# Optimization experiments

Hardware: AMD Instinct MI355X
Metric: run time of the kernel (lower is better)

The kernel has to match this reference:

```python
import jax, jax.numpy as jnp
import numpy as np

B, C, H, W = 16, 1024, 64, 64
NODE_H, NODE_W = 32, 32
N = NODE_H * NODE_W          # 1024 nodes
HID = 16                     # hidden_ch


def setup_inputs() -> dict:
    key = jax.random.key(0)
    k0, k1, k2 = jax.random.split(key, 3)
    feature = jax.random.normal(k0, (B, C, H, W), dtype=jnp.float32)
    mu_w = jax.random.normal(k1, (HID, C, 3, 3), dtype=jnp.float32) * 0.02
    mu_b = jnp.zeros((HID,), dtype=jnp.float32)
    lv_w = jax.random.normal(k2, (HID, C, 1, 1), dtype=jnp.float32) * 0.02
    lv_b = jnp.zeros((HID,), dtype=jnp.float32)
    return {"feature": feature, "mu_w": mu_w, "mu_b": mu_b, "lv_w": lv_w, "lv_b": lv_b}


def _conv(x, w, b, pad):
    y = jax.lax.conv_general_dilated(
        x, w, window_strides=(1, 1), padding=pad,
        dimension_numbers=("NCHW", "OIHW", "NCHW"))
    return y + b[None, :, None, None]


def reference(feature, mu_w, mu_b, lv_w, lv_b):
    # AdaptiveAvgPool2d((32,32)) with H,W multiples of 32 == mean over 2x2 blocks
    nodes = feature.reshape(B, C, NODE_H, H // NODE_H, NODE_W, W // NODE_W).mean(axis=(3, 5))
    mu = _conv(nodes, mu_w, mu_b, "SAME")      # (B, HID, 32, 32), Dropout is identity at eval
    log_var = _conv(nodes, lv_w, lv_b, "VALID")  # 1x1 conv, pad 0

    # eval-mode reparameterize: z = mu; torch raw reshape (B,HID,32,32)->(B,N,HID)
    z = mu.reshape(B, N, HID)

    kl_loss = -(0.5 * N * HID) * jnp.mean(
        jnp.sum(1.0 + 2.0 * log_var - mu ** 2 - jnp.exp(log_var) ** 2, axis=1))

    A = jnp.einsum("bnc,bmc->bnm", z, z)       # (B, N, N)
    A = jax.nn.relu(A)
    Ad = jnp.diagonal(A, axis1=1, axis2=2)      # (B, N)
    sigma = jnp.sum(Ad, axis=1)                 # (B,)
    gamma = jnp.sqrt(1.0 + N / (sigma + 1e-7))[:, None, None]  # (B,1,1)
    dl_loss = -gamma * jnp.log(Ad + 1e-7).sum() / (B * N * N)  # (B,1,1), faithful to torch

    eye = jnp.eye(N, dtype=A.dtype)
    A = A + gamma * (Ad[:, :, None] * eye)      # batched diagflat scatter

    # Laplacian normalize with self loop
    A = A + eye[None]
    deg_inv_sqrt = (jnp.sum(A, axis=1) + 1e-5) ** -0.5          # (B, N)
    LA = deg_inv_sqrt[:, :, None] * A * deg_inv_sqrt[:, None, :]

    z_hat = mu.reshape(B, N, HID) * (1.0 - log_var.reshape(B, N, HID))
    z_hat = gamma * z_hat
    return (LA, z, z_hat, kl_loss, dl_loss)
```

## Files before the change

kernel.cpp:

```cpp
#include <hip/hip_runtime.h>

typedef short short8 __attribute__((ext_vector_type(8)));
typedef float f32x4 __attribute__((ext_vector_type(4)));
typedef unsigned short ushort4v __attribute__((ext_vector_type(4)));

#define ZOFF   16777216
#define ZHOFF  17039360
#define KLOFF  17301504
#define DLOFF  17301505
#define APK_U  16777216
#define LVPK_U 16924672
#define AD_W   0
#define DIS_W  16384
#define PART_W 32768
#define GAM_W  34816
#define PMU_W  65536
#define PLV_W  2162688
#define Z16F   3211264

__device__ __forceinline__ unsigned short f2bf(float f) {
    unsigned int u = __float_as_uint(f);
    unsigned int r = (u + 0x7fffu + ((u >> 16) & 1u)) >> 16;
    return (unsigned short)r;
}
__device__ __forceinline__ float bf2f(unsigned short u) {
    return __uint_as_float(((unsigned int)u) << 16);
}

__global__ __launch_bounds__(256) void pool_tr_kernel(const float* __restrict__ f,
        unsigned short* __restrict__ nT, const float* __restrict__ mu_w,
        const float* __restrict__ lv_w, unsigned short* __restrict__ apk,
        unsigned short* __restrict__ lvpk)
{
    __shared__ float pls[64 * 35];
    int blk = blockIdx.x;
    int b  = blk >> 9;
    int y  = (blk >> 4) & 31;
    int cb = blk & 15;
    int t  = threadIdx.x;
    int rr  = (t >> 4) & 1;
    int c16 = t & 15;
    int cho = t >> 5;
    #pragma unroll
    for (int k = 0; k < 8; ++k) {
        int ch = (k << 3) + cho;
        float4 v = ((const float4*)f)[
            ((((b << 10) + (cb << 6) + ch) << 6) + (y << 1) + rr) * 16 + c16];
        float h0 = v.x + v.y, h1 = v.z + v.w;
        float g0 = h0 + __shfl_xor(h0, 16);
        float g1 = h1 + __shfl_xor(h1, 16);
        if (rr == 0) {
            pls[ch * 35 + (c16 << 1)]     = 0.25f * g0;
            pls[ch * 35 + (c16 << 1) + 1] = 0.25f * g1;
        }
    }
    __syncthreads();
    int px = t >> 3, cg2 = t & 7;
    unsigned short o8[8];
    #pragma unroll
    for (int i = 0; i < 8; ++i) o8[i] = f2bf(pls[((cg2 << 3) + i) * 35 + px]);
    int ofs = ((((b << 10) + (y << 5) + px)) << 10) + (cb << 6) + (cg2 << 3);
    *(short8*)&nT[ofs] = *(short8*)o8;

    if (blk < 640) {
        int idx = blk * 256 + t;
        if (idx < 147456) {
            int tap = idx >> 14;
            int rem = idx & 16383;
            int ks = rem >> 9;
            int lane = (rem >> 3) & 63;
            int j = idx & 7;
            int o = lane & 15;
            int cc = (ks << 5) + ((lane >> 4) << 3) + j;
            apk[idx] = f2bf(mu_w[((o << 10) + cc) * 9 + tap]);
        } else {
            int i2 = idx - 147456;
            int ks = i2 >> 9;
            int lane = (i2 >> 3) & 63;
            int j = i2 & 7;
            int o = lane & 15;
            int cc = (ks << 5) + ((lane >> 4) << 3) + j;
            lvpk[i2] = f2bf(lv_w[(o << 10) + cc]);
        }
    }
}

__global__ __launch_bounds__(256) void conv_mfma(const unsigned short* __restrict__ nT,
        const unsigned short* __restrict__ apk, const unsigned short* __restrict__ lvpk,
        unsigned short* __restrict__ pmu, unsigned short* __restrict__ plv)
{
    __shared__ unsigned short st[6 * 34 * 40];
    int blk = blockIdx.x;
    int b  = blk >> 6;
    int yt = (blk >> 3) & 7;
    int kc = blk & 7;
    int y0 = yt << 2;
    int t  = threadIdx.x;
    int w  = t >> 6, l = t & 63;
    int px = l & 15, chg = l >> 4;
    f32x4 accm[2] = {{0,0,0,0},{0,0,0,0}};
    f32x4 accv[2] = {{0,0,0,0},{0,0,0,0}};

    if (t < 48) {
        int row = t >> 3, side = (t >> 2) & 1, quarter = t & 3;
        short8 z8 = {0,0,0,0,0,0,0,0};
        *(short8*)&st[(row * 34 + side * 33) * 40 + quarter * 8] = z8;
    }

    for (int s = 0; s < 4; ++s) {
        int ksg = (kc << 2) + s;
        int cs  = ksg << 5;
        __syncthreads();
        #pragma unroll
        for (int k2 = 0; k2 < 3; ++k2) {
            int q = t + (k2 << 8);
            int quarter = q & 3, x = (q >> 2) & 31, row = q >> 7;
            int yin = y0 - 1 + row;
            short8 v = {0,0,0,0,0,0,0,0};
            if (yin >= 0 && yin < 32)
                v = *(const short8*)&nT[(((b << 10) + (yin << 5) + x) << 10) + cs + quarter * 8];
            *(short8*)&st[(row * 34 + x + 1) * 40 + quarter * 8] = v;
        }
        __syncthreads();
        short8 bw[9], bvw;
        #pragma unroll
        for (int tap = 0; tap < 9; ++tap)
            bw[tap] = *(const short8*)&apk[((tap << 5) + ksg) * 512 + l * 8];
        bvw = *(const short8*)&lvpk[(ksg << 9) + l * 8];
        #pragma unroll
        for (int h = 0; h < 2; ++h) {
            short8 actr;
            #pragma unroll
            for (int ky = 0; ky < 3; ++ky) {
                int row = w + ky;
                #pragma unroll
                for (int kx = 0; kx < 3; ++kx) {
                    int xx = (h << 4) + px + kx;
                    short8 a = *(const short8*)&st[(row * 34 + xx) * 40 + chg * 8];
                    if (ky == 1 && kx == 1) actr = a;
                    accm[h] = __builtin_amdgcn_mfma_f32_16x16x32_bf16(a, bw[ky*3+kx], accm[h], 0, 0, 0);
                }
            }
            accv[h] = __builtin_amdgcn_mfma_f32_16x16x32_bf16(actr, bvw, accv[h], 0, 0, 0);
        }
    }
    int o = px;
    #pragma unroll
    for (int h = 0; h < 2; ++h) {
        int x = (h << 4) + (chg << 2);
        int idx = (((kc << 4) + b) << 14) + (o << 10) + ((y0 + w) << 5) + x;
        ushort4v m16, v16;
        #pragma unroll
        for (int j = 0; j < 4; ++j) { m16[j] = f2bf(accm[h][j]); v16[j] = f2bf(accv[h][j]); }
        *(ushort4v*)&pmu[idx] = m16;
        *(ushort4v*)&plv[idx] = v16;
    }
}

__global__ __launch_bounds__(256) void stats_kernel(const unsigned short* __restrict__ pmu,
        const unsigned short* __restrict__ plv, const float* __restrict__ mu_b,
        const float* __restrict__ lv_b, float* __restrict__ z,
        float* __restrict__ lvout, float* __restrict__ ws)
{
    __shared__ float smu[16 * 68], slv[16 * 68];
    __shared__ float red[3][4];
    unsigned short* z16 = (unsigned short*)(ws + Z16F);
    int blk = blockIdx.x;
    int b = blk >> 4, ng = blk & 15;
    int t = threadIdx.x;
    {
        int o = t >> 4, f4c = t & 15;
        int base = (b << 14) + (o << 10) + (ng << 6) + (f4c << 2);
        f32x4 m = {0,0,0,0}, lv = {0,0,0,0};
        #pragma unroll
        for (int kc = 0; kc < 8; ++kc) {
            ushort4v mu16 = *(const ushort4v*)(pmu + (kc << 18) + base);
            ushort4v lv16 = *(const ushort4v*)(plv + (kc << 18) + base);
            #pragma unroll
            for (int c = 0; c < 4; ++c) {
                m[c]  += bf2f(mu16[c]);
                lv[c] += bf2f(lv16[c]);
            }
        }
        float mb = mu_b[o], lb = lv_b[o];
        #pragma unroll
        for (int c = 0; c < 4; ++c) {
            smu[o * 68 + (f4c << 2) + c] = m[c] + mb;
            slv[o * 68 + (f4c << 2) + c] = lv[c] + lb;
        }
    }
    __syncthreads();
    int node2 = t >> 2, og = t & 3;
    f32x4 zm, zl;
    float ad = 0.f, klp = 0.f;
    #pragma unroll
    for (int c = 0; c < 4; ++c) {
        float mm = smu[((og << 2) + c) * 68 + node2];
        float ll = slv[((og << 2) + c) * 68 + node2];
        zm[c] = mm; zl[c] = ll;
        ad  += mm * mm;
        klp += 1.0f + 2.0f * ll - mm * mm - expf(2.0f * ll);
    }
    int zofs = (b << 14) + (((ng << 6) + node2) << 4) + (og << 2);
    *(f32x4*)(z + zofs)     = zm;
    *(f32x4*)(lvout + zofs) = zl;
    ushort4v z16v;
    #pragma unroll
    for (int c = 0; c < 4; ++c) z16v[c] = f2bf(zm[c]);
    *(ushort4v*)&z16[zofs] = z16v;
    ad  += __shfl_xor(ad, 1);  ad  += __shfl_xor(ad, 2);
    klp += __shfl_xor(klp, 1); klp += __shfl_xor(klp, 2);
    float lg = logf(ad + 1e-7f);
    if (og == 0) ws[AD_W + (b << 10) + (ng << 6) + node2] = ad;
    float sgc = (og == 0) ? ad  : 0.f;
    float klc = (og == 0) ? klp : 0.f;
    float lgc = (og == 0) ? lg  : 0.f;
    #pragma unroll
    for (int off = 32; off > 0; off >>= 1) {
        sgc += __shfl_down(sgc, off);
        klc += __shfl_down(klc, off);
        lgc += __shfl_down(lgc, off);
    }
    int wv = t >> 6;
    if ((t & 63) == 0) { red[0][wv] = sgc; red[1][wv] = klc; red[2][wv] = lgc; }
    __syncthreads();
    if (t == 0) {
        ws[PART_W + (blk << 2) + 0] = red[0][0] + red[0][1] + red[0][2] + red[0][3];
        ws[PART_W + (blk << 2) + 1] = red[1][0] + red[1][1] + red[1][2] + red[1][3];
        ws[PART_W + (blk << 2) + 2] = red[2][0] + red[2][1] + red[2][2] + red[2][3];
    }
}

__global__ __launch_bounds__(256) void deg_kernel(const float* __restrict__ z,
        float* __restrict__ lvzh, float* __restrict__ ws, float* __restrict__ out)
{
    __shared__ float psum[16][17];
    __shared__ float redk[4], redl[4], fin[2];
    int b  = blockIdx.x >> 6;
    int n0 = (blockIdx.x & 63) * 16;
    int t  = threadIdx.x;
    int nl = t & 15;
    int mg = t >> 4;
    float sg16 = 0.f;
    #pragma unroll
    for (int g = 0; g < 16; ++g) sg16 += ws[PART_W + (((b << 4) + g) << 2)];
    float gam = sqrtf(1.0f + 1024.0f / (sg16 + 1e-7f));
    const float* zb = z + (b << 14);
    const float4* a4 = (const float4*)(zb + (n0 + nl) * 16);
    float4 a0 = a4[0], a1 = a4[1], a2 = a4[2], a3 = a4[3];
    float rs = 0.f;
    const float4* m4 = (const float4*)(zb + (mg << 6) * 16);
    for (int m = 0; m < 64; ++m) {
        float4 s0 = m4[m*4], s1 = m4[m*4+1], s2 = m4[m*4+2], s3 = m4[m*4+3];
        float d = a0.x*s0.x + a0.y*s0.y + a0.z*s0.z + a0.w*s0.w
                + a1.x*s1.x + a1.y*s1.y + a1.z*s1.z + a1.w*s1.w
                + a2.x*s2.x + a2.y*s2.y + a2.z*s2.z + a2.w*s2.w
                + a3.x*s3.x + a3.y*s3.y + a3.z*s3.z + a3.w*s3.w;
        rs += fmaxf(d, 0.f);
    }
    psum[mg][nl] = rs;
    __syncthreads();
    if (t < 16) {
        float total = 0.f;
        #pragma unroll
        for (int gg = 0; gg < 16; ++gg) total += psum[gg][t];
        int n = n0 + t;
        float deg = total + gam * ws[AD_W + (b << 10) + n] + 1.0f;
        ws[DIS_W + (b << 10) + n] = rsqrtf(deg + 1e-5f);
    }
    int zi = (b << 14) + ((n0 + (t >> 4)) << 4) + (t & 15);
    lvzh[zi] = gam * z[zi] * (1.0f - lvzh[zi]);
    if (blockIdx.x == 0) {
        float kl = ws[PART_W + (t << 2) + 1];
        float lg = ws[PART_W + (t << 2) + 2];
        #pragma unroll
        for (int off = 32; off > 0; off >>= 1) {
            kl += __shfl_down(kl, off);
            lg += __shfl_down(lg, off);
        }
        if ((t & 63) == 0) { redk[t >> 6] = kl; redl[t >> 6] = lg; }
        __syncthreads();
        if (t == 0) {
            fin[0] = redk[0] + redk[1] + redk[2] + redk[3];
            fin[1] = redl[0] + redl[1] + redl[2] + redl[3];
            out[KLOFF] = -0.5f * fin[0];
        }
        __syncthreads();
        if (t < 16) {
            float s = 0.f;
            #pragma unroll
            for (int g = 0; g < 16; ++g) s += ws[PART_W + (((t << 4) + g) << 2)];
            float gm = sqrtf(1.0f + 1024.0f / (s + 1e-7f));
            ws[GAM_W + t] = gm;
            out[DLOFF + t] = -gm * fin[1] / 16777216.0f;
        }
    }
}

__global__ __launch_bounds__(256) void la_kernel(const float* __restrict__ ws,
        float* __restrict__ LA)
{
    __shared__ float dan[64], dbm[64], sAd[64];
    const unsigned short* z16 = (const unsigned short*)(ws + Z16F);
    int b    = blockIdx.x >> 8;
    int tile = blockIdx.x & 255;
    int n0 = (tile >> 4) * 64;
    int m0 = (tile & 15) * 64;
    int t  = threadIdx.x;
    int w  = t >> 6, l = t & 63;
    const float* dis = ws + DIS_W + (b << 10);
    if (t < 64)       dan[t]      = dis[n0 + t];
    else if (t < 128) dbm[t - 64] = dis[m0 + (t - 64)];
    else if (t < 192) sAd[t - 128] = (n0 == m0) ? ws[AD_W + (b << 10) + n0 + (t - 128)] : 0.0f;
    __syncthreads();
    float g = ws[GAM_W + b];
    const unsigned short* zb = z16 + (b << 14);
    int rn = n0 + (w << 4);
    int lo = l & 15, hi = l >> 4;
    short8 afrag = {0,0,0,0,0,0,0,0};
    if (l < 32) afrag = *(const short8*)&zb[((rn + lo) << 4) + (hi << 3)];
    #pragma unroll
    for (int j = 0; j < 4; ++j) {
        int rm = m0 + (j << 4);
        short8 bfrag = {0,0,0,0,0,0,0,0};
        if (l < 32) bfrag = *(const short8*)&zb[((rm + lo) << 4) + (hi << 3)];
        f32x4 d = {0.f, 0.f, 0.f, 0.f};
        d = __builtin_amdgcn_mfma_f32_16x16x32_bf16(afrag, bfrag, d, 0, 0, 0);
        int c = rm + lo;
        float dm = dbm[(j << 4) + lo];
        #pragma unroll
        for (int jj = 0; jj < 4; ++jj) {
            int r = rn + (hi << 2) + jj;
            float v = fmaxf(d[jj], 0.f);
            if (r == c) v += g * sAd[r - n0] + 1.0f;
            float dn = dan[(w << 4) + (hi << 2) + jj];
            LA[((size_t)b << 20) + ((size_t)r << 10) + c] = dn * dm * v;
        }
    }
}

extern "C" void kernel_launch(void* const* d_in, const int* in_sizes, int n_in,
                              void* d_out, int out_size, void* d_ws, size_t ws_size,
                              hipStream_t stream) {
    const float* feature = (const float*)d_in[0];
    const float* mu_w    = (const float*)d_in[1];
    const float* mu_b    = (const float*)d_in[2];
    const float* lv_w    = (const float*)d_in[3];
    const float* lv_b    = (const float*)d_in[4];
    float* out = (float*)d_out;
    float* ws  = (float*)d_ws;
    unsigned short* nT   = (unsigned short*)d_out;
    unsigned short* apk  = nT + APK_U;
    unsigned short* lvpk = nT + LVPK_U;
    unsigned short* pmu16 = (unsigned short*)(ws + PMU_W);
    unsigned short* plv16 = (unsigned short*)(ws + PLV_W);

    pool_tr_kernel<<<8192, 256, 0, stream>>>(feature, nT, mu_w, lv_w, apk, lvpk);
    conv_mfma<<<1024, 256, 0, stream>>>(nT, apk, lvpk, pmu16, plv16);
    stats_kernel<<<256, 256, 0, stream>>>(pmu16, plv16, mu_b, lv_b,
                                          out + ZOFF, out + ZHOFF, ws);
    deg_kernel<<<1024, 256, 0, stream>>>(out + ZOFF, out + ZHOFF, ws, out);
    la_kernel<<<4096, 256, 0, stream>>>(ws, out);
}
```

Baseline: 128.4 us.

## Compute degree row sums with bf16 MFMA instead of scalar fp32 dot products

The degree kernel now computes relu(z·zᵀ) row sums using 16x16x32 bf16 MFMA on a bf16 copy of z held in the workspace. The 16-wide hidden dimension is padded to K=32 by zeroing half the lanes, and partial sums are reduced with xor shuffles. Each block now covers 64 rows using 4 waves, so the grid shrinks from 1024 to 256 blocks. The intent is to replace the heavy scalar FMA loop with matrix-core work, at the cost of bf16 rounding in the degree values.

Result: faster. 111.7 us (-13.0%).

```diff
diff --git a/kernel.cpp b/kernel.cpp
--- a/kernel.cpp
+++ b/kernel.cpp
@@ -234,43 +234,51 @@
 __global__ __launch_bounds__(256) void deg_kernel(const float* __restrict__ z,
         float* __restrict__ lvzh, float* __restrict__ ws, float* __restrict__ out)
 {
-    __shared__ float psum[16][17];
     __shared__ float redk[4], redl[4], fin[2];
-    int b  = blockIdx.x >> 6;
-    int n0 = (blockIdx.x & 63) * 16;
+    const unsigned short* z16 = (const unsigned short*)(ws + Z16F);
+    int blk = blockIdx.x;
+    int b  = blk >> 4;
+    int n0 = (blk & 15) << 6;
     int t  = threadIdx.x;
-    int nl = t & 15;
-    int mg = t >> 4;
+    int w  = t >> 6, l = t & 63;
+    int lo = l & 15, hi = l >> 4;
     float sg16 = 0.f;
     #pragma unroll
     for (int g = 0; g < 16; ++g) sg16 += ws[PART_W + (((b << 4) + g) << 2)];
     float gam = sqrtf(1.0f + 1024.0f / (sg16 + 1e-7f));
-    const float* zb = z + (b << 14);
-    const float4* a4 = (const float4*)(zb + (n0 + nl) * 16);
-    float4 a0 = a4[0], a1 = a4[1], a2 = a4[2], a3 = a4[3];
-    float rs = 0.f;
-    const float4* m4 = (const float4*)(zb + (mg << 6) * 16);
-    for (int m = 0; m < 64; ++m) {
-        float4 s0 = m4[m*4], s1 = m4[m*4+1], s2 = m4[m*4+2], s3 = m4[m*4+3];
-        float d = a0.x*s0.x + a0.y*s0.y + a0.z*s0.z + a0.w*s0.w
-                + a1.x*s1.x + a1.y*s1.y + a1.z*s1.z + a1.w*s1.w
-                + a2.x*s2.x + a2.y*s2.y + a2.z*s2.z + a2.w*s2.w
-                + a3.x*s3.x + a3.y*s3.y + a3.z*s3.z + a3.w*s3.w;
-        rs += fmaxf(d, 0.f);
-    }
-    psum[mg][nl] = rs;
-    __syncthreads();
-    if (t < 16) {
-        float total = 0.f;
-        #pragma unroll
-        for (int gg = 0; gg < 16; ++gg) total += psum[gg][t];
-        int n = n0 + t;
-        float deg = total + gam * ws[AD_W + (b << 10) + n] + 1.0f;
-        ws[DIS_W + (b << 10) + n] = rsqrtf(deg + 1e-5f);
-    }
-    int zi = (b << 14) + ((n0 + (t >> 4)) << 4) + (t & 15);
-    lvzh[zi] = gam * z[zi] * (1.0f - lvzh[zi]);
-    if (blockIdx.x == 0) {
+    #pragma unroll
+    for (int e = 0; e < 4; ++e) {
+        int zi = (b << 14) + (n0 << 4) + (e << 8) + t;
+        lvzh[zi] = gam * z[zi] * (1.0f - lvzh[zi]);
+    }
+    const unsigned short* zb = z16 + (b << 14);
+    int rn = n0 + (w << 4);
+    short8 afrag = {0,0,0,0,0,0,0,0};
+    if (l < 32) afrag = *(const short8*)&zb[((rn + lo) << 4) + (hi << 3)];
+    f32x4 rs = {0.f, 0.f, 0.f, 0.f};
+    #pragma unroll 4
+    for (int mt = 0; mt < 64; ++mt) {
+        short8 bfrag = {0,0,0,0,0,0,0,0};
+        if (l < 32) bfrag = *(const short8*)&zb[(((mt << 4) + lo) << 4) + (hi << 3)];
+        f32x4 d = {0.f, 0.f, 0.f, 0.f};
+        d = __builtin_amdgcn_mfma_f32_16x16x32_bf16(afrag, bfrag, d, 0, 0, 0);
+        #pragma unroll
+        for (int jj = 0; jj < 4; ++jj) rs[jj] += fmaxf(d[jj], 0.f);
+    }
+    #pragma unroll
+    for (int m = 1; m < 16; m <<= 1) {
+        #pragma unroll
+        for (int jj = 0; jj < 4; ++jj) rs[jj] += __shfl_xor(rs[jj], m);
+    }
+    if (lo == 0) {
+        #pragma unroll
+        for (int jj = 0; jj < 4; ++jj) {
+            int n = rn + (hi << 2) + jj;
+            float deg = rs[jj] + gam * ws[AD_W + (b << 10) + n] + 1.0f;
+            ws[DIS_W + (b << 10) + n] = rsqrtf(deg + 1e-5f);
+        }
+    }
+    if (blk == 0) {
         float kl = ws[PART_W + (t << 2) + 1];
         float lg = ws[PART_W + (t << 2) + 2];
         #pragma unroll
@@ -359,6 +367,6 @@
     conv_mfma<<<1024, 256, 0, stream>>>(nT, apk, lvpk, pmu16, plv16);
     stats_kernel<<<256, 256, 0, stream>>>(pmu16, plv16, mu_b, lv_b,
                                           out + ZOFF, out + ZHOFF, ws);
-    deg_kernel<<<1024, 256, 0, stream>>>(out + ZOFF, out + ZHOFF, ws, out);
+    deg_kernel<<<256, 256, 0, stream>>>(out + ZOFF, out + ZHOFF, ws, out);
     la_kernel<<<4096, 256, 0, stream>>>(ws, out);
 }
```
